# Kernel tuning notes

Measured on AMD Instinct MI355X. Metric: run time of the kernel, lower is better.

## Reference

```python
import jax, jax.numpy as jnp
import numpy as np

N_P, N_A = 100000, 20000
F_P, D_A, H = 512, 128, 256
E_W, E_C = 200000, 400000


def setup_inputs() -> dict:
    key = jax.random.key(0)
    ks = jax.random.split(key, 32)
    s = 0.05  # param init scale
    inp = {
        # node inputs
        'paper_feat': (jax.random.uniform(ks[0], (N_P, F_P)) < 0.02).astype(jnp.float32),  # sparse multi-hot
        'author_emb': jax.random.normal(ks[1], (N_A, D_A), jnp.float32),
        # edges: author --writes--> paper, paper --cites--> paper
        'writes_src': jax.random.randint(ks[2], (E_W,), 0, N_A, jnp.int32),
        'writes_dst': jax.random.randint(ks[3], (E_W,), 0, N_P, jnp.int32),
        'writes_w': jax.random.uniform(ks[4], (E_W,), jnp.float32),
        'cites_src': jax.random.randint(ks[5], (E_C,), 0, N_P, jnp.int32),
        'cites_dst': jax.random.randint(ks[6], (E_C,), 0, N_P, jnp.int32),
        'cites_w': jax.random.uniform(ks[7], (E_C,), jnp.float32),
        # layer 1 params (in dims per node type: paper=F_P, author=D_A)
        'W1_self_p': jax.random.normal(ks[8], (F_P, H), jnp.float32) * s,
        'b1_self_p': jnp.zeros((H,), jnp.float32),
        'W1_self_a': jax.random.normal(ks[9], (D_A, H), jnp.float32) * s,
        'b1_self_a': jnp.zeros((H,), jnp.float32),
        'W1_rel_writes': jax.random.normal(ks[10], (D_A, H), jnp.float32) * s,
        'b1_rel_writes': jnp.zeros((H,), jnp.float32),
        'W1_rel_cites': jax.random.normal(ks[11], (F_P, H), jnp.float32) * s,
        'b1_rel_cites': jnp.zeros((H,), jnp.float32),
        # layer 2 params (all in dims = H)
        'W2_self_p': jax.random.normal(ks[12], (H, H), jnp.float32) * s,
        'b2_self_p': jnp.zeros((H,), jnp.float32),
        'W2_self_a': jax.random.normal(ks[13], (H, H), jnp.float32) * s,
        'b2_self_a': jnp.zeros((H,), jnp.float32),
        'W2_rel_writes': jax.random.normal(ks[14], (H, H), jnp.float32) * s,
        'b2_rel_writes': jnp.zeros((H,), jnp.float32),
        'W2_rel_cites': jax.random.normal(ks[15], (H, H), jnp.float32) * s,
        'b2_rel_cites': jnp.zeros((H,), jnp.float32),
    }
    return inp


def _hetero_layer(xp, xa, edges, Wsp, bsp, Wsa, bsa, Wrw, brw, Wrc, brc, activation):
    """One HeteroLayer: per-type self linear + per-relation gather/scale/scatter-add."""
    writes_src, writes_dst, writes_w, cites_src, cites_dst, cites_w = edges
    out_p = xp @ Wsp + bsp          # [N_P, H]
    out_a = xa @ Wsa + bsa          # [N_A, H]
    # relation author --writes--> paper
    msg_w = xa @ Wrw + brw          # dense per-relation linear on source nodes
    gathered_w = msg_w[writes_src] * writes_w[:, None]          # gather + edge weight
    out_p = out_p + jax.ops.segment_sum(gathered_w, writes_dst, num_segments=out_p.shape[0])
    # relation paper --cites--> paper
    msg_c = xp @ Wrc + brc
    gathered_c = msg_c[cites_src] * cites_w[:, None]
    out_p = out_p + jax.ops.segment_sum(gathered_c, cites_dst, num_segments=out_p.shape[0])
    if activation:
        out_p = jax.nn.elu(out_p)
        out_a = jax.nn.elu(out_a)
    return out_p, out_a


def reference(paper_feat, author_emb,
              writes_src, writes_dst, writes_w,
              cites_src, cites_dst, cites_w,
              W1_self_p, b1_self_p, W1_self_a, b1_self_a,
              W1_rel_writes, b1_rel_writes, W1_rel_cites, b1_rel_cites,
              W2_self_p, b2_self_p, W2_self_a, b2_self_a,
              W2_rel_writes, b2_rel_writes, W2_rel_cites, b2_rel_cites):
    edges = (writes_src, writes_dst, writes_w, cites_src, cites_dst, cites_w)
    xp, xa = _hetero_layer(paper_feat, author_emb, edges,
                           W1_self_p, b1_self_p, W1_self_a, b1_self_a,
                           W1_rel_writes, b1_rel_writes, W1_rel_cites, b1_rel_cites,
                           activation=True)
    xp, xa = _hetero_layer(xp, xa, edges,
                           W2_self_p, b2_self_p, W2_self_a, b2_self_a,
                           W2_rel_writes, b2_rel_writes, W2_rel_cites, b2_rel_cites,
                           activation=False)
    return xp, xa
```

## Files before the change

### kernel.cpp

```cpp
#include <hip/hip_runtime.h>
#include <cstdint>
#include <cstddef>

constexpr int Hd  = 256;
constexpr int N_P = 100000;
constexpr int N_A = 20000;
constexpr int F_P = 512;
constexpr int D_A = 128;

typedef short bf16x8 __attribute__((ext_vector_type(8)));
typedef float f32x4  __attribute__((ext_vector_type(4)));

__device__ __forceinline__ unsigned short f2b(float x) {
    unsigned u = __float_as_uint(x);
    u += 0x7fffu + ((u >> 16) & 1u);
    return (unsigned short)(u >> 16);
}
__device__ __forceinline__ float b2f(unsigned short h) {
    return __uint_as_float((unsigned)h << 16);
}

__device__ __forceinline__ void bsplit(float x, unsigned short& hi, unsigned short& lo) {
    const unsigned u = __float_as_uint(x);
    hi = (unsigned short)(u >> 16);
    const float r = x - __uint_as_float(u & 0xffff0000u);
    lo = (unsigned short)(__float_as_uint(r) >> 16);
}

__global__ void prep_kernel(const float* __restrict__ W1sa, const float* __restrict__ W1rw,
                            const float* __restrict__ W2sa, const float* __restrict__ W2rw,
                            const float* __restrict__ W2rc, const float* __restrict__ W2sp,
                            const float* __restrict__ W1rc,
                            const float* __restrict__ b1sa, const float* __restrict__ b1rw,
                            const float* __restrict__ b2sa, const float* __restrict__ b2rw,
                            const float* __restrict__ b2rc, const float* __restrict__ b2sp,
                            unsigned short* __restrict__ w1h,  unsigned short* __restrict__ w1l,
                            unsigned short* __restrict__ wA2h, unsigned short* __restrict__ wA2l,
                            unsigned short* __restrict__ wP2h, unsigned short* __restrict__ wP2l,
                            unsigned short* __restrict__ wcb,
                            float* __restrict__ bc1, float* __restrict__ bcA2,
                            float* __restrict__ bcP2) {
    const int b = blockIdx.x;
    if (b < 640) {
        const float *Wa, *Wb; unsigned short *wh, *wl; int rel;
        if (b < 128)      { Wa = W1sa; Wb = W1rw; wh = w1h;  wl = w1l;  rel = b; }
        else if (b < 384) { Wa = W2sa; Wb = W2rw; wh = wA2h; wl = wA2l; rel = b - 128; }
        else              { Wa = W2rc; Wb = W2sp; wh = wP2h; wl = wP2l; rel = b - 384; }
        const int ks  = rel >> 5;
        const int nfg = rel & 31;
        const int l   = threadIdx.x;
        const float* W = (nfg < 16) ? Wa : Wb;
        const int col  = (nfg & 15) * 16 + (l & 15);
        const size_t base = ((size_t)rel * 64 + l) * 8;
        #pragma unroll
        for (int j = 0; j < 8; ++j) {
            const int k = ks * 32 + ((l >> 4) * 8) + j;
            unsigned short h, lw;
            bsplit(W[(size_t)k * Hd + col], h, lw);
            wh[base + j] = h;
            wl[base + j] = lw;
        }
    } else if (b < 896) {
        const int i0 = (b - 640) * 512 + threadIdx.x * 8;
        #pragma unroll
        for (int j = 0; j < 8; ++j) wcb[i0 + j] = f2b(W1rc[i0 + j]);
    } else {
        const int t     = (b - 896) * 64 + threadIdx.x;
        const int which = t >> 9;
        const int idx   = t & 511;
        const float* src; float* dst;
        if (which == 0)      { src = (idx < 256) ? b1sa : b1rw; dst = bc1; }
        else if (which == 1) { src = (idx < 256) ? b2sa : b2rw; dst = bcA2; }
        else                 { src = (idx < 256) ? b2rc : b2sp; dst = bcP2; }
        dst[idx] = src[idx & 255];
    }
}

template<int ABF>
__global__ void mfma_dual_kernel(const void* __restrict__ Av, const int K,
                                 const unsigned short* __restrict__ whi,
                                 const unsigned short* __restrict__ wlo,
                                 const float* __restrict__ bcat,
                                 void* __restrict__ Oa, void* __restrict__ Ob,
                                 const int actA, const int actB,
                                 const int bfA, const int bfB) {
    extern __shared__ char smem[];
    char* sh = smem;
    char* sl = smem + 32 * K * 2;
    const int  tid = threadIdx.x;
    const int  wid = tid >> 6;
    const int  l   = tid & 63;
    const long m0  = (long)blockIdx.x * 32;
    const int  rowStride = 2 * K;

    const int kq4 = K >> 2;
    if constexpr (ABF) {
        const unsigned short* A = (const unsigned short*)Av;
        for (int i = tid; i < 32 * kq4; i += 256) {
            const int row = i / kq4;
            const int kq  = i - row * kq4;
            const ushort4 v = *(const ushort4*)(A + (m0 + row) * K + kq * 4);
            const int ofs = row * rowStride + ((kq * 8) ^ ((row & 7) << 4));
            *(ushort4*)(sh + ofs) = v;
        }
    } else {
        const float* A = (const float*)Av;
        for (int i = tid; i < 32 * kq4; i += 256) {
            const int row = i / kq4;
            const int kq  = i - row * kq4;
            const float4 v = *(const float4*)(A + (m0 + row) * K + kq * 4);
            unsigned short h0, h1, h2, h3, l0, l1, l2, l3;
            bsplit(v.x, h0, l0); bsplit(v.y, h1, l1);
            bsplit(v.z, h2, l2); bsplit(v.w, h3, l3);
            const int ofs = row * rowStride + ((kq * 8) ^ ((row & 7) << 4));
            *(ushort4*)(sh + ofs) = make_ushort4(h0, h1, h2, h3);
            *(ushort4*)(sl + ofs) = make_ushort4(l0, l1, l2, l3);
        }
    }
    __syncthreads();

    f32x4 acc[2][8];
    #pragma unroll
    for (int nf = 0; nf < 8; ++nf) {
        const float b = bcat[wid * 128 + nf * 16 + (l & 15)];
        acc[0][nf] = (f32x4){b, b, b, b};
        acc[1][nf] = (f32x4){b, b, b, b};
    }

    const int kb  = (l >> 4) * 16;
    const int r0  = l & 15;
    const int r1  = 16 + r0;
    const int sw  = (l & 7) << 4;
    const int ro0 = r0 * rowStride;
    const int ro1 = r1 * rowStride;
    for (int ks = 0; ks < (K >> 5); ++ks) {
        const int bk = (ks * 64 + kb) ^ sw;
        const bf16x8 ah0 = *(const bf16x8*)(sh + ro0 + bk);
        const bf16x8 ah1 = *(const bf16x8*)(sh + ro1 + bk);
        bf16x8 al0, al1;
        if constexpr (!ABF) {
            al0 = *(const bf16x8*)(sl + ro0 + bk);
            al1 = *(const bf16x8*)(sl + ro1 + bk);
        }
        const size_t wbase = (((size_t)ks * 32 + wid * 8) * 64 + l) * 8;
        #pragma unroll
        for (int nf = 0; nf < 8; ++nf) {
            const bf16x8 bh = *(const bf16x8*)(whi + wbase + (size_t)nf * 512);
            const bf16x8 bl = *(const bf16x8*)(wlo + wbase + (size_t)nf * 512);
            acc[0][nf] = __builtin_amdgcn_mfma_f32_16x16x32_bf16(ah0, bh, acc[0][nf], 0, 0, 0);
            acc[1][nf] = __builtin_amdgcn_mfma_f32_16x16x32_bf16(ah1, bh, acc[1][nf], 0, 0, 0);
            if constexpr (!ABF) {
                acc[0][nf] = __builtin_amdgcn_mfma_f32_16x16x32_bf16(al0, bh, acc[0][nf], 0, 0, 0);
                acc[1][nf] = __builtin_amdgcn_mfma_f32_16x16x32_bf16(al1, bh, acc[1][nf], 0, 0, 0);
            }
            acc[0][nf] = __builtin_amdgcn_mfma_f32_16x16x32_bf16(ah0, bl, acc[0][nf], 0, 0, 0);
            acc[1][nf] = __builtin_amdgcn_mfma_f32_16x16x32_bf16(ah1, bl, acc[1][nf], 0, 0, 0);
        }
    }

    #pragma unroll
    for (int mf = 0; mf < 2; ++mf) {
        #pragma unroll
        for (int nf = 0; nf < 8; ++nf) {
            const int colg = wid * 128 + nf * 16 + (l & 15);
            void* O;
            int col, act, isbf;
            if (colg < 256) { O = Oa; col = colg;       act = actA; isbf = bfA; }
            else            { O = Ob; col = colg - 256; act = actB; isbf = bfB; }
            const long row = m0 + mf * 16 + ((l >> 4) * 4);
            const f32x4 v = acc[mf][nf];
            #pragma unroll
            for (int r = 0; r < 4; ++r) {
                float x = v[r];
                if (act) x = x > 0.f ? x : expm1f(x);
                if (isbf) ((unsigned short*)O)[(row + r) * Hd + col] = f2b(x);
                else      ((float*)O)[(row + r) * Hd + col] = x;
            }
        }
    }
}

__global__ void __launch_bounds__(256, 2)
sparse_dual_kernel(const float* __restrict__ pf,
                   const float* __restrict__ Ws, const float* __restrict__ bs,
                   const unsigned short* __restrict__ Wc, const float* __restrict__ bc,
                   unsigned short* __restrict__ outS, unsigned short* __restrict__ outC) {
    __shared__ unsigned short q[4][176];
    const int lane = threadIdx.x & 63;
    const int wid  = threadIdx.x >> 6;
    const long r0  = (long)blockIdx.x * 16 + wid * 4;
    unsigned short* wq = q[wid];

    const float4* p0 = (const float4*)(pf + (r0 + 0) * F_P);
    const float4* p1 = (const float4*)(pf + (r0 + 1) * F_P);
    const float4* p2 = (const float4*)(pf + (r0 + 2) * F_P);
    const float4* p3 = (const float4*)(pf + (r0 + 3) * F_P);
    const float4 A0 = p0[lane], B0 = p0[64 + lane];
    const float4 A1 = p1[lane], B1 = p1[64 + lane];
    const float4 A2 = p2[lane], B2 = p2[64 + lane];
    const float4 A3 = p3[lane], B3 = p3[64 + lane];

    int qn = 0;
#define SP_GRP(VAL, KOFS, ROW) { \
    const bool nz = (VAL) != 0.f; \
    const unsigned long long mk = __ballot(nz); \
    if (nz) { \
        const int within = __builtin_amdgcn_mbcnt_hi((unsigned)(mk >> 32), \
                           __builtin_amdgcn_mbcnt_lo((unsigned)mk, 0)); \
        wq[qn + within] = (unsigned short)(((KOFS) + lane * 4) | ((ROW) << 9)); \
    } \
    qn += (int)__popcll(mk); }
    SP_GRP(A0.x, 0,   0) SP_GRP(A0.y, 1,   0) SP_GRP(A0.z, 2,   0) SP_GRP(A0.w, 3,   0)
    SP_GRP(B0.x, 256, 0) SP_GRP(B0.y, 257, 0) SP_GRP(B0.z, 258, 0) SP_GRP(B0.w, 259, 0)
    SP_GRP(A1.x, 0,   1) SP_GRP(A1.y, 1,   1) SP_GRP(A1.z, 2,   1) SP_GRP(A1.w, 3,   1)
    SP_GRP(B1.x, 256, 1) SP_GRP(B1.y, 257, 1) SP_GRP(B1.z, 258, 1) SP_GRP(B1.w, 259, 1)
    SP_GRP(A2.x, 0,   2) SP_GRP(A2.y, 1,   2) SP_GRP(A2.z, 2,   2) SP_GRP(A2.w, 3,   2)
    SP_GRP(B2.x, 256, 2) SP_GRP(B2.y, 257, 2) SP_GRP(B2.z, 258, 2) SP_GRP(B2.w, 259, 2)
    SP_GRP(A3.x, 0,   3) SP_GRP(A3.y, 1,   3) SP_GRP(A3.z, 2,   3) SP_GRP(A3.w, 3,   3)
    SP_GRP(B3.x, 256, 3) SP_GRP(B3.y, 257, 3) SP_GRP(B3.z, 258, 3) SP_GRP(B3.w, 259, 3)
#undef SP_GRP
    int qnp = (qn + 7) & ~7;
    if (qnp == 0) qnp = 8;
    if (lane < qnp - qn) wq[qn + lane] = 0x0800;
    __syncthreads();

    float4 aS0, aC0;
    { const float4 bsv = ((const float4*)bs)[lane]; aS0 = bsv; }
    { const float4 bcv = ((const float4*)bc)[lane]; aC0 = bcv; }
    float4 aS1 = aS0, aS2 = aS0, aS3 = aS0;
    float4 aC1 = aC0, aC2 = aC0, aC3 = aC0;

#define DEC1(EV, K, R, P) { const int e_ = __builtin_amdgcn_readfirstlane((int)(EV)); \
    K = e_ & 511; R = (e_ >> 9) & 3; P = e_ >> 11; }
#define ISS1(S4, C4, K) { \
    S4 = ((const float4*)(Ws + ((size_t)(K) << 8)))[lane]; \
    C4 = ((const ushort4*)(Wc + ((size_t)(K) << 8)))[lane]; }
#define ACC1(S4, C4, R, P) if (!(P)) { \
    if ((R) == 0)      { aS0.x += S4.x; aS0.y += S4.y; aS0.z += S4.z; aS0.w += S4.w; \
                         aC0.x += b2f(C4.x); aC0.y += b2f(C4.y); aC0.z += b2f(C4.z); aC0.w += b2f(C4.w); } \
    else if ((R) == 1) { aS1.x += S4.x; aS1.y += S4.y; aS1.z += S4.z; aS1.w += S4.w; \
                         aC1.x += b2f(C4.x); aC1.y += b2f(C4.y); aC1.z += b2f(C4.z); aC1.w += b2f(C4.w); } \
    else if ((R) == 2) { aS2.x += S4.x; aS2.y += S4.y; aS2.z += S4.z; aS2.w += S4.w; \
                         aC2.x += b2f(C4.x); aC2.y += b2f(C4.y); aC2.z += b2f(C4.z); aC2.w += b2f(C4.w); } \
    else               { aS3.x += S4.x; aS3.y += S4.y; aS3.z += S4.z; aS3.w += S4.w; \
                         aC3.x += b2f(C4.x); aC3.y += b2f(C4.y); aC3.z += b2f(C4.z); aC3.w += b2f(C4.w); } }

    const int nch = qnp >> 2;
    int kA0, kA1, kA2, kA3, rA0, rA1, rA2, rA3, pA0, pA1, pA2, pA3;
    int kB0, kB1, kB2, kB3, rB0, rB1, rB2, rB3, pB0, pB1, pB2, pB3;
    float4  sA0, sA1, sA2, sA3, sB0, sB1, sB2, sB3;
    ushort4 cA0, cA1, cA2, cA3, cB0, cB1, cB2, cB3;

    ushort4 qv = *(const ushort4*)(wq + 0);
    DEC1(qv.x, kA0, rA0, pA0) DEC1(qv.y, kA1, rA1, pA1)
    DEC1(qv.z, kA2, rA2, pA2) DEC1(qv.w, kA3, rA3, pA3)
    ISS1(sA0, cA0, kA0) ISS1(sA1, cA1, kA1) ISS1(sA2, cA2, kA2) ISS1(sA3, cA3, kA3)
    qv = *(const ushort4*)(wq + 4);
    DEC1(qv.x, kB0, rB0, pB0) DEC1(qv.y, kB1, rB1, pB1)
    DEC1(qv.z, kB2, rB2, pB2) DEC1(qv.w, kB3, rB3, pB3)
    ISS1(sB0, cB0, kB0) ISS1(sB1, cB1, kB1) ISS1(sB2, cB2, kB2) ISS1(sB3, cB3, kB3)

    for (int c = 0; c + 2 < nch; c += 2) {
        qv = *(const ushort4*)(wq + 4 * (c + 2));
        ACC1(sA0, cA0, rA0, pA0) ACC1(sA1, cA1, rA1, pA1)
        ACC1(sA2, cA2, rA2, pA2) ACC1(sA3, cA3, rA3, pA3)
        DEC1(qv.x, kA0, rA0, pA0) DEC1(qv.y, kA1, rA1, pA1)
        DEC1(qv.z, kA2, rA2, pA2) DEC1(qv.w, kA3, rA3, pA3)
        ISS1(sA0, cA0, kA0) ISS1(sA1, cA1, kA1) ISS1(sA2, cA2, kA2) ISS1(sA3, cA3, kA3)
        qv = *(const ushort4*)(wq + 4 * (c + 3));
        ACC1(sB0, cB0, rB0, pB0) ACC1(sB1, cB1, rB1, pB1)
        ACC1(sB2, cB2, rB2, pB2) ACC1(sB3, cB3, rB3, pB3)
        DEC1(qv.x, kB0, rB0, pB0) DEC1(qv.y, kB1, rB1, pB1)
        DEC1(qv.z, kB2, rB2, pB2) DEC1(qv.w, kB3, rB3, pB3)
        ISS1(sB0, cB0, kB0) ISS1(sB1, cB1, kB1) ISS1(sB2, cB2, kB2) ISS1(sB3, cB3, kB3)
    }
    ACC1(sA0, cA0, rA0, pA0) ACC1(sA1, cA1, rA1, pA1)
    ACC1(sA2, cA2, rA2, pA2) ACC1(sA3, cA3, rA3, pA3)
    ACC1(sB0, cB0, rB0, pB0) ACC1(sB1, cB1, rB1, pB1)
    ACC1(sB2, cB2, rB2, pB2) ACC1(sB3, cB3, rB3, pB3)
#undef DEC1
#undef ISS1
#undef ACC1

    ((ushort4*)(outS + (r0 + 0) * Hd))[lane] = make_ushort4(f2b(aS0.x), f2b(aS0.y), f2b(aS0.z), f2b(aS0.w));
    ((ushort4*)(outS + (r0 + 1) * Hd))[lane] = make_ushort4(f2b(aS1.x), f2b(aS1.y), f2b(aS1.z), f2b(aS1.w));
    ((ushort4*)(outS + (r0 + 2) * Hd))[lane] = make_ushort4(f2b(aS2.x), f2b(aS2.y), f2b(aS2.z), f2b(aS2.w));
    ((ushort4*)(outS + (r0 + 3) * Hd))[lane] = make_ushort4(f2b(aS3.x), f2b(aS3.y), f2b(aS3.z), f2b(aS3.w));
    ((ushort4*)(outC + (r0 + 0) * Hd))[lane] = make_ushort4(f2b(aC0.x), f2b(aC0.y), f2b(aC0.z), f2b(aC0.w));
    ((ushort4*)(outC + (r0 + 1) * Hd))[lane] = make_ushort4(f2b(aC1.x), f2b(aC1.y), f2b(aC1.z), f2b(aC1.w));
    ((ushort4*)(outC + (r0 + 2) * Hd))[lane] = make_ushort4(f2b(aC2.x), f2b(aC2.y), f2b(aC2.z), f2b(aC2.w));
    ((ushort4*)(outC + (r0 + 3) * Hd))[lane] = make_ushort4(f2b(aC3.x), f2b(aC3.y), f2b(aC3.z), f2b(aC3.w));
}

__global__ void hist_kernel(const int* __restrict__ wdst, const int EW,
                            const int* __restrict__ cdst, const int EC,
                            int* __restrict__ cnt) {
    for (int i = blockIdx.x * blockDim.x + threadIdx.x; i < EW + EC; i += gridDim.x * blockDim.x) {
        const int d = (i < EW) ? wdst[i] : cdst[i - EW];
        atomicAdd(&cnt[d], 1);
    }
}

__global__ void scan1_kernel(int* __restrict__ data, const int n, int* __restrict__ bsum) {
    __shared__ int s[256];
    const int t = threadIdx.x;
    const int base = blockIdx.x * 1024 + t * 4;
    int v0 = (base + 0 < n) ? data[base + 0] : 0;
    int v1 = (base + 1 < n) ? data[base + 1] : 0;
    int v2 = (base + 2 < n) ? data[base + 2] : 0;
    int v3 = (base + 3 < n) ? data[base + 3] : 0;
    const int tsum = v0 + v1 + v2 + v3;
    s[t] = tsum;
    __syncthreads();
    for (int off = 1; off < 256; off <<= 1) {
        int y = (t >= off) ? s[t - off] : 0;
        __syncthreads();
        if (t >= off) s[t] += y;
        __syncthreads();
    }
    const int e = s[t] - tsum;
    if (base + 0 < n) data[base + 0] = e;
    if (base + 1 < n) data[base + 1] = e + v0;
    if (base + 2 < n) data[base + 2] = e + v0 + v1;
    if (base + 3 < n) data[base + 3] = e + v0 + v1 + v2;
    if (t == 255) bsum[blockIdx.x] = s[255];
}

__global__ void scan2_kernel(int* __restrict__ bsum, const int nb) {
    __shared__ int s[256];
    const int t = threadIdx.x;
    const int v = (t < nb) ? bsum[t] : 0;
    s[t] = v;
    __syncthreads();
    for (int off = 1; off < 256; off <<= 1) {
        int y = (t >= off) ? s[t - off] : 0;
        __syncthreads();
        if (t >= off) s[t] += y;
        __syncthreads();
    }
    if (t < nb) bsum[t] = s[t] - v;
}

__global__ void scan3_kernel(int* __restrict__ data, const int n, const int* __restrict__ bsum) {
    const int i = blockIdx.x * blockDim.x + threadIdx.x;
    if (i < n) data[i] += bsum[i >> 10];
}

__global__ void fill_kernel(const int* __restrict__ wsrc, const int* __restrict__ wdst,
                            const float* __restrict__ ww, const int EW,
                            const int* __restrict__ csrc, const int* __restrict__ cdst,
                            const float* __restrict__ cw, const int EC,
                            int* __restrict__ cur, int2* __restrict__ edges) {
    for (int i = blockIdx.x * blockDim.x + threadIdx.x; i < EW + EC; i += gridDim.x * blockDim.x) {
        int d, sp; float w;
        if (i < EW) { d = wdst[i]; sp = wsrc[i]; w = ww[i]; }
        else        { const int j = i - EW; d = cdst[j]; sp = N_A + csrc[j]; w = cw[j]; }
        const int p = atomicAdd(&cur[d], 1);
        edges[p] = make_int2(sp, __float_as_int(w));
    }
}

struct AgChunk { ushort4 g0, g1, g2, g3; float w0, w1, w2, w3; };

__device__ __forceinline__ void ag_issue(const int2* __restrict__ eq, const int base, const int n,
                                         const unsigned short* __restrict__ msg,
                                         const int lane, AgChunk& C) {
#define AG_ONE(J, GG, WW) { \
    const int idx = base + (J); \
    const int2 ee = eq[min(idx, n - 1)]; \
    WW = (idx < n) ? __int_as_float(ee.y) : 0.f; \
    GG = ((const ushort4*)(msg + (size_t)ee.x * Hd))[lane]; }
    AG_ONE(0, C.g0, C.w0)
    AG_ONE(1, C.g1, C.w1)
    AG_ONE(2, C.g2, C.w2)
    AG_ONE(3, C.g3, C.w3)
#undef AG_ONE
}

__device__ __forceinline__ void ag_acc(const AgChunk& C, float4& acc) {
#define AG_A(GG, WW) { \
    acc.x = fmaf(WW, b2f(GG.x), acc.x); acc.y = fmaf(WW, b2f(GG.y), acc.y); \
    acc.z = fmaf(WW, b2f(GG.z), acc.z); acc.w = fmaf(WW, b2f(GG.w), acc.w); }
    AG_A(C.g0, C.w0) AG_A(C.g1, C.w1) AG_A(C.g2, C.w2) AG_A(C.g3, C.w3)
#undef AG_A
}

template<int IOBF>
__global__ void aggregate_kernel(void* __restrict__ iov,
                                 const unsigned short* __restrict__ msgAll,
                                 const int* __restrict__ off,
                                 const int2* __restrict__ edges,
                                 const int do_elu) {
    __shared__ int2 eq[1024];
    const int wid  = threadIdx.x >> 6;
    const int lane = threadIdx.x & 63;
    const int p0   = blockIdx.x * 4;
    const int sAll = (p0 == 0) ? 0 : off[p0 - 1];
    const int tot  = off[p0 + 3] - sAll;
    const bool fits = (tot <= 1024);
    if (fits)
        for (int i = threadIdx.x; i < tot; i += 256) eq[i] = edges[sAll + i];
    __syncthreads();

    const int p = p0 + wid;
    const int s = (p == 0) ? 0 : off[p - 1];
    const int e = off[p];
    const int n = e - s;

    float4 acc;
    if constexpr (IOBF) {
        const ushort4 t = ((const ushort4*)((const unsigned short*)iov + (size_t)p * Hd))[lane];
        acc = make_float4(b2f(t.x), b2f(t.y), b2f(t.z), b2f(t.w));
    } else {
        acc = ((const float4*)((const float*)iov + (size_t)p * Hd))[lane];
    }

    if (n > 0) {
        if (fits) {
            const int2* eqw = eq + (s - sAll);
            int nc = (n + 3) >> 2;
            nc += (nc & 1);
            AgChunk CA, CB;
            ag_issue(eqw, 0, n, msgAll, lane, CA);
            int c = 1;
            for (; c + 1 < nc; c += 2) {
                ag_issue(eqw, 4 * c, n, msgAll, lane, CB);
                ag_acc(CA, acc);
                ag_issue(eqw, 4 * (c + 1), n, msgAll, lane, CA);
                ag_acc(CB, acc);
            }
            ag_issue(eqw, 4 * (nc - 1), n, msgAll, lane, CB);
            ag_acc(CA, acc);
            ag_acc(CB, acc);
        } else {
            for (int i = s; i < e; ++i) {
                const int2 ee = edges[i];
                const ushort4 g = ((const ushort4*)(msgAll + (size_t)ee.x * Hd))[lane];
                const float w = __int_as_float(ee.y);
                acc.x = fmaf(w, b2f(g.x), acc.x); acc.y = fmaf(w, b2f(g.y), acc.y);
                acc.z = fmaf(w, b2f(g.z), acc.z); acc.w = fmaf(w, b2f(g.w), acc.w);
            }
        }
    }
    if (do_elu) {
        acc.x = acc.x > 0.f ? acc.x : expm1f(acc.x);
        acc.y = acc.y > 0.f ? acc.y : expm1f(acc.y);
        acc.z = acc.z > 0.f ? acc.z : expm1f(acc.z);
        acc.w = acc.w > 0.f ? acc.w : expm1f(acc.w);
    }
    if constexpr (IOBF) {
        ((ushort4*)((unsigned short*)iov + (size_t)p * Hd))[lane] =
            make_ushort4(f2b(acc.x), f2b(acc.y), f2b(acc.z), f2b(acc.w));
    } else {
        ((float4*)((float*)iov + (size_t)p * Hd))[lane] = acc;
    }
}

extern "C" void kernel_launch(void* const* d_in, const int* in_sizes, int n_in,
                              void* d_out, int out_size, void* d_ws, size_t ws_size,
                              hipStream_t stream) {
    const float* pf    = (const float*)d_in[0];
    const float* ae    = (const float*)d_in[1];
    const int*   wsrc  = (const int*)d_in[2];
    const int*   wdst  = (const int*)d_in[3];
    const float* ww    = (const float*)d_in[4];
    const int*   csrc  = (const int*)d_in[5];
    const int*   cdst  = (const int*)d_in[6];
    const float* cw    = (const float*)d_in[7];
    const float* W1sp  = (const float*)d_in[8];
    const float* b1sp  = (const float*)d_in[9];
    const float* W1sa  = (const float*)d_in[10];
    const float* b1sa  = (const float*)d_in[11];
    const float* W1rw  = (const float*)d_in[12];
    const float* b1rw  = (const float*)d_in[13];
    const float* W1rc  = (const float*)d_in[14];
    const float* b1rc  = (const float*)d_in[15];
    const float* W2sp  = (const float*)d_in[16];
    const float* b2sp  = (const float*)d_in[17];
    const float* W2sa  = (const float*)d_in[18];
    const float* b2sa  = (const float*)d_in[19];
    const float* W2rw  = (const float*)d_in[20];
    const float* b2rw  = (const float*)d_in[21];
    const float* W2rc  = (const float*)d_in[22];
    const float* b2rc  = (const float*)d_in[23];

    const int E_W = in_sizes[2];
    const int E_C = in_sizes[5];

    float* outP = (float*)d_out;
    float* outA = outP + (size_t)N_P * Hd;

    float*          xa1    = (float*)d_ws;
    unsigned short* xp1b   = (unsigned short*)(xa1 + (size_t)N_A * Hd);
    unsigned short* msgAll = xp1b + (size_t)N_P * Hd;
    unsigned short* msgP   = msgAll + (size_t)N_A * Hd;
    int*            off    = (int*)(msgAll + (size_t)(N_A + N_P) * Hd);
    int2*           edges  = (int2*)(off + N_P);
    int*            bsum   = (int*)(edges + (E_W + E_C));
    float*          bc1    = (float*)(bsum + 256);
    float*          bcA2   = bc1 + 512;
    float*          bcP2   = bcA2 + 512;
    unsigned short* w1h    = (unsigned short*)(bcP2 + 512);
    unsigned short* w1l    = w1h  + (size_t)128 * 512;
    unsigned short* wA2h   = w1l  + (size_t)128 * 512;
    unsigned short* wA2l   = wA2h + (size_t)256 * 512;
    unsigned short* wP2h   = wA2l + (size_t)256 * 512;
    unsigned short* wP2l   = wP2h + (size_t)256 * 512;
    unsigned short* wcb    = wP2l + (size_t)256 * 512;

    const dim3 blk(256);
    const int  nb = (N_P + 1023) / 1024;

    prep_kernel<<<920, 64, 0, stream>>>(W1sa, W1rw, W2sa, W2rw, W2rc, W2sp, W1rc,
                                        b1sa, b1rw, b2sa, b2rw, b2rc, b2sp,
                                        w1h, w1l, wA2h, wA2l, wP2h, wP2l, wcb,
                                        bc1, bcA2, bcP2);

    hipMemsetAsync(off, 0, (size_t)N_P * sizeof(int), stream);
    hist_kernel<<<1024, blk, 0, stream>>>(wdst, E_W, cdst, E_C, off);
    scan1_kernel<<<nb, blk, 0, stream>>>(off, N_P, bsum);
    scan2_kernel<<<1,  blk, 0, stream>>>(bsum, nb);
    scan3_kernel<<<(N_P + 255) / 256, blk, 0, stream>>>(off, N_P, bsum);
    fill_kernel<<<1024, blk, 0, stream>>>(wsrc, wdst, ww, E_W, csrc, cdst, cw, E_C,
                                          off, edges);

    sparse_dual_kernel<<<N_P / 16, blk, 0, stream>>>(pf, W1sp, b1sp, wcb, b1rc,
                                                     xp1b, msgP);
    mfma_dual_kernel<0><<<N_A / 32, blk, 32 * 128 * 4, stream>>>(ae, 128, w1h, w1l, bc1,
                                                                 xa1, msgAll, 1, 0, 0, 1);
    aggregate_kernel<1><<<N_P / 4, blk, 0, stream>>>(xp1b, msgAll, off, edges, 1);

    mfma_dual_kernel<0><<<N_A / 32, blk, 32 * 256 * 4, stream>>>(xa1, 256, wA2h, wA2l, bcA2,
                                                                 outA, msgAll, 0, 0, 0, 1);
    mfma_dual_kernel<1><<<N_P / 32, blk, 32 * 256 * 2, stream>>>(xp1b, 256, wP2h, wP2l, bcP2,
                                                                 msgP, outP, 0, 0, 1, 0);
    aggregate_kernel<0><<<N_P / 4, blk, 0, stream>>>(outP, msgAll, off, edges, 0);
}
```

Before: 528.2 us.

## Replace sparse gather layer-1 paper transform with dense bf16 MFMA GEMM

Drops the ballot-based sparse accumulation kernel for the multi-hot paper features and computes the paper self and cites transforms as a dense 100000x512x512 GEMM on MFMA. The input is truncated to bf16, which is exact because the features are only 0 or 1, and only the high bf16 weight half is used. Weights for this GEMM are pre-swizzled into the MFMA layout in the prep kernel. This does dense work on roughly 98% zeros in exchange for regular matrix-core throughput, and the W1_self_p weights now enter as bf16 instead of fp32.

```diff
diff --git a/kernel.cpp b/kernel.cpp
--- a/kernel.cpp
+++ b/kernel.cpp
@@ -30,17 +30,19 @@
 __global__ void prep_kernel(const float* __restrict__ W1sa, const float* __restrict__ W1rw,
                             const float* __restrict__ W2sa, const float* __restrict__ W2rw,
                             const float* __restrict__ W2rc, const float* __restrict__ W2sp,
-                            const float* __restrict__ W1rc,
+                            const float* __restrict__ W1sp, const float* __restrict__ W1rc,
                             const float* __restrict__ b1sa, const float* __restrict__ b1rw,
                             const float* __restrict__ b2sa, const float* __restrict__ b2rw,
                             const float* __restrict__ b2rc, const float* __restrict__ b2sp,
+                            const float* __restrict__ b1sp, const float* __restrict__ b1rc,
                             unsigned short* __restrict__ w1h,  unsigned short* __restrict__ w1l,
                             unsigned short* __restrict__ wA2h, unsigned short* __restrict__ wA2l,
                             unsigned short* __restrict__ wP2h, unsigned short* __restrict__ wP2l,
-                            unsigned short* __restrict__ wcb,
+                            unsigned short* __restrict__ wP1h,
                             float* __restrict__ bc1, float* __restrict__ bcA2,
-                            float* __restrict__ bcP2) {
+                            float* __restrict__ bcP2, float* __restrict__ bcP1) {
     const int b = blockIdx.x;
+    const int l = threadIdx.x;
     if (b < 640) {
         const float *Wa, *Wb; unsigned short *wh, *wl; int rel;
         if (b < 128)      { Wa = W1sa; Wb = W1rw; wh = w1h;  wl = w1l;  rel = b; }
@@ -48,7 +50,6 @@
         else              { Wa = W2rc; Wb = W2sp; wh = wP2h; wl = wP2l; rel = b - 384; }
         const int ks  = rel >> 5;
         const int nfg = rel & 31;
-        const int l   = threadIdx.x;
         const float* W = (nfg < 16) ? Wa : Wb;
         const int col  = (nfg & 15) * 16 + (l & 15);
         const size_t base = ((size_t)rel * 64 + l) * 8;
@@ -60,18 +61,27 @@
             wh[base + j] = h;
             wl[base + j] = lw;
         }
-    } else if (b < 896) {
-        const int i0 = (b - 640) * 512 + threadIdx.x * 8;
+    } else if (b < 1152) {
+        const int rel = b - 640;
+        const int ks  = rel >> 5;
+        const int nfg = rel & 31;
+        const float* W = (nfg < 16) ? W1sp : W1rc;
+        const int col  = (nfg & 15) * 16 + (l & 15);
+        const size_t base = ((size_t)rel * 64 + l) * 8;
         #pragma unroll
-        for (int j = 0; j < 8; ++j) wcb[i0 + j] = f2b(W1rc[i0 + j]);
+        for (int j = 0; j < 8; ++j) {
+            const int k = ks * 32 + ((l >> 4) * 8) + j;
+            wP1h[base + j] = f2b(W[(size_t)k * Hd + col]);
+        }
     } else {
-        const int t     = (b - 896) * 64 + threadIdx.x;
+        const int t     = (b - 1152) * 64 + l;
         const int which = t >> 9;
         const int idx   = t & 511;
         const float* src; float* dst;
-        if (which == 0)      { src = (idx < 256) ? b1sa : b1rw; dst = bc1; }
+        if (which == 0)      { src = (idx < 256) ? b1sa : b1rw; dst = bc1;  }
         else if (which == 1) { src = (idx < 256) ? b2sa : b2rw; dst = bcA2; }
-        else                 { src = (idx < 256) ? b2rc : b2sp; dst = bcP2; }
+        else if (which == 2) { src = (idx < 256) ? b2rc : b2sp; dst = bcP2; }
+        else                 { src = (idx < 256) ? b1sp : b1rc; dst = bcP1; }
         dst[idx] = src[idx & 255];
     }
 }
@@ -94,7 +104,7 @@
     const int  rowStride = 2 * K;
 
     const int kq4 = K >> 2;
-    if constexpr (ABF) {
+    if constexpr (ABF == 1) {
         const unsigned short* A = (const unsigned short*)Av;
         for (int i = tid; i < 32 * kq4; i += 256) {
             const int row = i / kq4;
@@ -102,6 +112,20 @@
             const ushort4 v = *(const ushort4*)(A + (m0 + row) * K + kq * 4);
             const int ofs = row * rowStride + ((kq * 8) ^ ((row & 7) << 4));
             *(ushort4*)(sh + ofs) = v;
+        }
+    } else if constexpr (ABF == 2) {
+        const float* A = (const float*)Av;
+        for (int i = tid; i < 32 * kq4; i += 256) {
+            const int row = i / kq4;
+            const int kq  = i - row * kq4;
+            const float4 v = *(const float4*)(A + (m0 + row) * K + kq * 4);
+            const ushort4 h = make_ushort4(
+                (unsigned short)(__float_as_uint(v.x) >> 16),
+                (unsigned short)(__float_as_uint(v.y) >> 16),
+                (unsigned short)(__float_as_uint(v.z) >> 16),
+                (unsigned short)(__float_as_uint(v.w) >> 16));
+            const int ofs = row * rowStride + ((kq * 8) ^ ((row & 7) << 4));
+            *(ushort4*)(sh + ofs) = h;
         }
     } else {
         const float* A = (const float*)Av;
@@ -138,7 +162,7 @@
         const bf16x8 ah0 = *(const bf16x8*)(sh + ro0 + bk);
         const bf16x8 ah1 = *(const bf16x8*)(sh + ro1 + bk);
         bf16x8 al0, al1;
-        if constexpr (!ABF) {
+        if constexpr (ABF == 0) {
             al0 = *(const bf16x8*)(sl + ro0 + bk);
             al1 = *(const bf16x8*)(sl + ro1 + bk);
         }
@@ -146,15 +170,17 @@
         #pragma unroll
         for (int nf = 0; nf < 8; ++nf) {
             const bf16x8 bh = *(const bf16x8*)(whi + wbase + (size_t)nf * 512);
-            const bf16x8 bl = *(const bf16x8*)(wlo + wbase + (size_t)nf * 512);
             acc[0][nf] = __builtin_amdgcn_mfma_f32_16x16x32_bf16(ah0, bh, acc[0][nf], 0, 0, 0);
             acc[1][nf] = __builtin_amdgcn_mfma_f32_16x16x32_bf16(ah1, bh, acc[1][nf], 0, 0, 0);
-            if constexpr (!ABF) {
+            if constexpr (ABF == 0) {
                 acc[0][nf] = __builtin_amdgcn_mfma_f32_16x16x32_bf16(al0, bh, acc[0][nf], 0, 0, 0);
                 acc[1][nf] = __builtin_amdgcn_mfma_f32_16x16x32_bf16(al1, bh, acc[1][nf], 0, 0, 0);
             }
-            acc[0][nf] = __builtin_amdgcn_mfma_f32_16x16x32_bf16(ah0, bl, acc[0][nf], 0, 0, 0);
-            acc[1][nf] = __builtin_amdgcn_mfma_f32_16x16x32_bf16(ah1, bl, acc[1][nf], 0, 0, 0);
+            if constexpr (ABF != 2) {
+                const bf16x8 bl = *(const bf16x8*)(wlo + wbase + (size_t)nf * 512);
+                acc[0][nf] = __builtin_amdgcn_mfma_f32_16x16x32_bf16(ah0, bl, acc[0][nf], 0, 0, 0);
+                acc[1][nf] = __builtin_amdgcn_mfma_f32_16x16x32_bf16(ah1, bl, acc[1][nf], 0, 0, 0);
+            }
         }
     }
 
@@ -178,118 +204,6 @@
             }
         }
     }
-}
-
-__global__ void __launch_bounds__(256, 2)
-sparse_dual_kernel(const float* __restrict__ pf,
-                   const float* __restrict__ Ws, const float* __restrict__ bs,
-                   const unsigned short* __restrict__ Wc, const float* __restrict__ bc,
-                   unsigned short* __restrict__ outS, unsigned short* __restrict__ outC) {
-    __shared__ unsigned short q[4][176];
-    const int lane = threadIdx.x & 63;
-    const int wid  = threadIdx.x >> 6;
-    const long r0  = (long)blockIdx.x * 16 + wid * 4;
-    unsigned short* wq = q[wid];
-
-    const float4* p0 = (const float4*)(pf + (r0 + 0) * F_P);
-    const float4* p1 = (const float4*)(pf + (r0 + 1) * F_P);
-    const float4* p2 = (const float4*)(pf + (r0 + 2) * F_P);
-    const float4* p3 = (const float4*)(pf + (r0 + 3) * F_P);
-    const float4 A0 = p0[lane], B0 = p0[64 + lane];
-    const float4 A1 = p1[lane], B1 = p1[64 + lane];
-    const float4 A2 = p2[lane], B2 = p2[64 + lane];
-    const float4 A3 = p3[lane], B3 = p3[64 + lane];
-
-    int qn = 0;
-#define SP_GRP(VAL, KOFS, ROW) { \
-    const bool nz = (VAL) != 0.f; \
-    const unsigned long long mk = __ballot(nz); \
-    if (nz) { \
-        const int within = __builtin_amdgcn_mbcnt_hi((unsigned)(mk >> 32), \
-                           __builtin_amdgcn_mbcnt_lo((unsigned)mk, 0)); \
-        wq[qn + within] = (unsigned short)(((KOFS) + lane * 4) | ((ROW) << 9)); \
-    } \
-    qn += (int)__popcll(mk); }
-    SP_GRP(A0.x, 0,   0) SP_GRP(A0.y, 1,   0) SP_GRP(A0.z, 2,   0) SP_GRP(A0.w, 3,   0)
-    SP_GRP(B0.x, 256, 0) SP_GRP(B0.y, 257, 0) SP_GRP(B0.z, 258, 0) SP_GRP(B0.w, 259, 0)
-    SP_GRP(A1.x, 0,   1) SP_GRP(A1.y, 1,   1) SP_GRP(A1.z, 2,   1) SP_GRP(A1.w, 3,   1)
-    SP_GRP(B1.x, 256, 1) SP_GRP(B1.y, 257, 1) SP_GRP(B1.z, 258, 1) SP_GRP(B1.w, 259, 1)
-    SP_GRP(A2.x, 0,   2) SP_GRP(A2.y, 1,   2) SP_GRP(A2.z, 2,   2) SP_GRP(A2.w, 3,   2)
-    SP_GRP(B2.x, 256, 2) SP_GRP(B2.y, 257, 2) SP_GRP(B2.z, 258, 2) SP_GRP(B2.w, 259, 2)
-    SP_GRP(A3.x, 0,   3) SP_GRP(A3.y, 1,   3) SP_GRP(A3.z, 2,   3) SP_GRP(A3.w, 3,   3)
-    SP_GRP(B3.x, 256, 3) SP_GRP(B3.y, 257, 3) SP_GRP(B3.z, 258, 3) SP_GRP(B3.w, 259, 3)
-#undef SP_GRP
-    int qnp = (qn + 7) & ~7;
-    if (qnp == 0) qnp = 8;
-    if (lane < qnp - qn) wq[qn + lane] = 0x0800;
-    __syncthreads();
-
-    float4 aS0, aC0;
-    { const float4 bsv = ((const float4*)bs)[lane]; aS0 = bsv; }
-    { const float4 bcv = ((const float4*)bc)[lane]; aC0 = bcv; }
-    float4 aS1 = aS0, aS2 = aS0, aS3 = aS0;
-    float4 aC1 = aC0, aC2 = aC0, aC3 = aC0;
-
-#define DEC1(EV, K, R, P) { const int e_ = __builtin_amdgcn_readfirstlane((int)(EV)); \
-    K = e_ & 511; R = (e_ >> 9) & 3; P = e_ >> 11; }
-#define ISS1(S4, C4, K) { \
-    S4 = ((const float4*)(Ws + ((size_t)(K) << 8)))[lane]; \
-    C4 = ((const ushort4*)(Wc + ((size_t)(K) << 8)))[lane]; }
-#define ACC1(S4, C4, R, P) if (!(P)) { \
-    if ((R) == 0)      { aS0.x += S4.x; aS0.y += S4.y; aS0.z += S4.z; aS0.w += S4.w; \
-                         aC0.x += b2f(C4.x); aC0.y += b2f(C4.y); aC0.z += b2f(C4.z); aC0.w += b2f(C4.w); } \
-    else if ((R) == 1) { aS1.x += S4.x; aS1.y += S4.y; aS1.z += S4.z; aS1.w += S4.w; \
-                         aC1.x += b2f(C4.x); aC1.y += b2f(C4.y); aC1.z += b2f(C4.z); aC1.w += b2f(C4.w); } \
-    else if ((R) == 2) { aS2.x += S4.x; aS2.y += S4.y; aS2.z += S4.z; aS2.w += S4.w; \
-                         aC2.x += b2f(C4.x); aC2.y += b2f(C4.y); aC2.z += b2f(C4.z); aC2.w += b2f(C4.w); } \
-    else               { aS3.x += S4.x; aS3.y += S4.y; aS3.z += S4.z; aS3.w += S4.w; \
-                         aC3.x += b2f(C4.x); aC3.y += b2f(C4.y); aC3.z += b2f(C4.z); aC3.w += b2f(C4.w); } }
-
-    const int nch = qnp >> 2;
-    int kA0, kA1, kA2, kA3, rA0, rA1, rA2, rA3, pA0, pA1, pA2, pA3;
-    int kB0, kB1, kB2, kB3, rB0, rB1, rB2, rB3, pB0, pB1, pB2, pB3;
-    float4  sA0, sA1, sA2, sA3, sB0, sB1, sB2, sB3;
-    ushort4 cA0, cA1, cA2, cA3, cB0, cB1, cB2, cB3;
-
-    ushort4 qv = *(const ushort4*)(wq + 0);
-    DEC1(qv.x, kA0, rA0, pA0) DEC1(qv.y, kA1, rA1, pA1)
-    DEC1(qv.z, kA2, rA2, pA2) DEC1(qv.w, kA3, rA3, pA3)
-    ISS1(sA0, cA0, kA0) ISS1(sA1, cA1, kA1) ISS1(sA2, cA2, kA2) ISS1(sA3, cA3, kA3)
-    qv = *(const ushort4*)(wq + 4);
-    DEC1(qv.x, kB0, rB0, pB0) DEC1(qv.y, kB1, rB1, pB1)
-    DEC1(qv.z, kB2, rB2, pB2) DEC1(qv.w, kB3, rB3, pB3)
-    ISS1(sB0, cB0, kB0) ISS1(sB1, cB1, kB1) ISS1(sB2, cB2, kB2) ISS1(sB3, cB3, kB3)
-
-    for (int c = 0; c + 2 < nch; c += 2) {
-        qv = *(const ushort4*)(wq + 4 * (c + 2));
-        ACC1(sA0, cA0, rA0, pA0) ACC1(sA1, cA1, rA1, pA1)
-        ACC1(sA2, cA2, rA2, pA2) ACC1(sA3, cA3, rA3, pA3)
-        DEC1(qv.x, kA0, rA0, pA0) DEC1(qv.y, kA1, rA1, pA1)
-        DEC1(qv.z, kA2, rA2, pA2) DEC1(qv.w, kA3, rA3, pA3)
-        ISS1(sA0, cA0, kA0) ISS1(sA1, cA1, kA1) ISS1(sA2, cA2, kA2) ISS1(sA3, cA3, kA3)
-        qv = *(const ushort4*)(wq + 4 * (c + 3));
-        ACC1(sB0, cB0, rB0, pB0) ACC1(sB1, cB1, rB1, pB1)
-        ACC1(sB2, cB2, rB2, pB2) ACC1(sB3, cB3, rB3, pB3)
-        DEC1(qv.x, kB0, rB0, pB0) DEC1(qv.y, kB1, rB1, pB1)
-        DEC1(qv.z, kB2, rB2, pB2) DEC1(qv.w, kB3, rB3, pB3)
-        ISS1(sB0, cB0, kB0) ISS1(sB1, cB1, kB1) ISS1(sB2, cB2, kB2) ISS1(sB3, cB3, kB3)
-    }
-    ACC1(sA0, cA0, rA0, pA0) ACC1(sA1, cA1, rA1, pA1)
-    ACC1(sA2, cA2, rA2, pA2) ACC1(sA3, cA3, rA3, pA3)
-    ACC1(sB0, cB0, rB0, pB0) ACC1(sB1, cB1, rB1, pB1)
-    ACC1(sB2, cB2, rB2, pB2) ACC1(sB3, cB3, rB3, pB3)
-#undef DEC1
-#undef ISS1
-#undef ACC1
-
-    ((ushort4*)(outS + (r0 + 0) * Hd))[lane] = make_ushort4(f2b(aS0.x), f2b(aS0.y), f2b(aS0.z), f2b(aS0.w));
-    ((ushort4*)(outS + (r0 + 1) * Hd))[lane] = make_ushort4(f2b(aS1.x), f2b(aS1.y), f2b(aS1.z), f2b(aS1.w));
-    ((ushort4*)(outS + (r0 + 2) * Hd))[lane] = make_ushort4(f2b(aS2.x), f2b(aS2.y), f2b(aS2.z), f2b(aS2.w));
-    ((ushort4*)(outS + (r0 + 3) * Hd))[lane] = make_ushort4(f2b(aS3.x), f2b(aS3.y), f2b(aS3.z), f2b(aS3.w));
-    ((ushort4*)(outC + (r0 + 0) * Hd))[lane] = make_ushort4(f2b(aC0.x), f2b(aC0.y), f2b(aC0.z), f2b(aC0.w));
-    ((ushort4*)(outC + (r0 + 1) * Hd))[lane] = make_ushort4(f2b(aC1.x), f2b(aC1.y), f2b(aC1.z), f2b(aC1.w));
-    ((ushort4*)(outC + (r0 + 2) * Hd))[lane] = make_ushort4(f2b(aC2.x), f2b(aC2.y), f2b(aC2.z), f2b(aC2.w));
-    ((ushort4*)(outC + (r0 + 3) * Hd))[lane] = make_ushort4(f2b(aC3.x), f2b(aC3.y), f2b(aC3.z), f2b(aC3.w));
 }
 
 __global__ void hist_kernel(const int* __restrict__ wdst, const int EW,
@@ -500,21 +414,22 @@
     float*          bc1    = (float*)(bsum + 256);
     float*          bcA2   = bc1 + 512;
     float*          bcP2   = bcA2 + 512;
-    unsigned short* w1h    = (unsigned short*)(bcP2 + 512);
+    float*          bcP1   = bcP2 + 512;
+    unsigned short* w1h    = (unsigned short*)(bcP1 + 512);
     unsigned short* w1l    = w1h  + (size_t)128 * 512;
     unsigned short* wA2h   = w1l  + (size_t)128 * 512;
     unsigned short* wA2l   = wA2h + (size_t)256 * 512;
     unsigned short* wP2h   = wA2l + (size_t)256 * 512;
     unsigned short* wP2l   = wP2h + (size_t)256 * 512;
-    unsigned short* wcb    = wP2l + (size_t)256 * 512;
+    unsigned short* wP1h   = wP2l + (size_t)256 * 512;
 
     const dim3 blk(256);
     const int  nb = (N_P + 1023) / 1024;
 
-    prep_kernel<<<920, 64, 0, stream>>>(W1sa, W1rw, W2sa, W2rw, W2rc, W2sp, W1rc,
-                                        b1sa, b1rw, b2sa, b2rw, b2rc, b2sp,
-                                        w1h, w1l, wA2h, wA2l, wP2h, wP2l, wcb,
-                                        bc1, bcA2, bcP2);
+    prep_kernel<<<1184, 64, 0, stream>>>(W1sa, W1rw, W2sa, W2rw, W2rc, W2sp, W1sp, W1rc,
+                                         b1sa, b1rw, b2sa, b2rw, b2rc, b2sp, b1sp, b1rc,
+                                         w1h, w1l, wA2h, wA2l, wP2h, wP2l, wP1h,
+                                         bc1, bcA2, bcP2, bcP1);
 
     hipMemsetAsync(off, 0, (size_t)N_P * sizeof(int), stream);
     hist_kernel<<<1024, blk, 0, stream>>>(wdst, E_W, cdst, E_C, off);
@@ -524,15 +439,15 @@
     fill_kernel<<<1024, blk, 0, stream>>>(wsrc, wdst, ww, E_W, csrc, cdst, cw, E_C,
                                           off, edges);
 
-    sparse_dual_kernel<<<N_P / 16, blk, 0, stream>>>(pf, W1sp, b1sp, wcb, b1rc,
-                                                     xp1b, msgP);
+    mfma_dual_kernel<2><<<N_P / 32, blk, 32 * 512 * 2, stream>>>(pf, 512, wP1h, wP1h, bcP1,
+                                                                 xp1b, msgP, 0, 0, 1, 1);
     mfma_dual_kernel<0><<<N_A / 32, blk, 32 * 128 * 4, stream>>>(ae, 128, w1h, w1l, bc1,
                                                                  xa1, msgAll, 1, 0, 0, 1);
     aggregate_kernel<1><<<N_P / 4, blk, 0, stream>>>(xp1b, msgAll, off, edges, 1);
 
     mfma_dual_kernel<0><<<N_A / 32, blk, 32 * 256 * 4, stream>>>(xa1, 256, wA2h, wA2l, bcA2,
                                                                  outA, msgAll, 0, 0, 0, 1);
-    mfma_dual_kernel<1><<<N_P / 32, blk, 32 * 256 * 2, stream>>>(xp1b, 256, wP2h, wP2l, bcP2,
+    mfma_dual_kernel<1><<<N_P / 32, blk, 32 * 256 * 4, stream>>>(xp1b, 256, wP2h, wP2l, bcP2,
                                                                  msgP, outP, 0, 0, 1, 0);
     aggregate_kernel<0><<<N_P / 4, blk, 0, stream>>>(outP, msgAll, off, edges, 0);
 }
```

Result: slower. 556.0 us (+5.3%).
